# Kernel optimization log

Measured on AMD Instinct MI355X. Metric: run time of the kernel, lower is better.

The kernel has to match this reference:

```python
import jax, jax.numpy as jnp
import numpy as np

B, S, D, P = 4, 2048, 1024, 1024

def setup_inputs() -> dict:
    key = jax.random.key(0)
    k1, k2, k3, k4 = jax.random.split(key, 4)
    x = jax.random.normal(k1, (B, S, D), dtype=jnp.float32)
    # nn.Linear weight is (out, in); store transposed (in, out) for x @ W
    scale = 1.0 / np.sqrt(D)
    Wq = jax.random.normal(k2, (D, P), dtype=jnp.float32) * scale
    Wk = jax.random.normal(k3, (D, P), dtype=jnp.float32) * scale
    Wv = jax.random.normal(k4, (D, P), dtype=jnp.float32) * scale
    return {"x": x, "Wq": Wq, "Wk": Wk, "Wv": Wv}

def reference(x, Wq, Wk, Wv):
    # projections (no bias)
    q = x @ Wq  # (B,S,P)
    k = x @ Wk
    v = x @ Wv
    scores = jnp.einsum('bsd,btd->bst', q, k)  # (B,S,S)
    seq = x.shape[1]
    causal = jnp.triu(jnp.ones((seq, seq), dtype=bool), k=1)
    scores = jnp.where(causal, -jnp.inf, scores)
    scores = scores / jnp.sqrt(jnp.asarray(P, dtype=scores.dtype))
    attn = jax.nn.softmax(scores, axis=-1)
    # dropout_prob=0.0 -> identity
    context = jnp.einsum('bst,btd->bsd', attn, v)  # (B,S,P)
    return context
```

## Files before the change

kernel.cpp:

```cpp
#include <hip/hip_runtime.h>
#include <hip/hip_bf16.h>


#define BDIM 4
#define SDIM 2048
#define DDIM 1024
#define PDIM 1024

typedef __attribute__((ext_vector_type(8))) short bf16x8;
typedef __attribute__((ext_vector_type(4))) float f32x4;

__device__ __forceinline__ unsigned short f2bf(float f) {
    union { float f; unsigned int u; } v; v.f = f;
    unsigned int u = v.u;
    unsigned int r = (u + 0x7fffu + ((u >> 16) & 1u)) >> 16;
    return (unsigned short)r;
}

__device__ __forceinline__ float bf2f(unsigned short h) {
    union { unsigned int u; float f; } v;
    v.u = ((unsigned int)h) << 16;
    return v.f;
}

__device__ __forceinline__ void async16(const unsigned short* g, unsigned short* l) {
    __builtin_amdgcn_global_load_lds(
        (const __attribute__((address_space(1))) unsigned int*)g,
        (__attribute__((address_space(3))) unsigned int*)l,
        16, 0, 0);
}

__device__ __forceinline__ void storeC(float* C, size_t idx, float v) { C[idx] = v; }
__device__ __forceinline__ void storeC(unsigned short* C, size_t idx, float v) { C[idx] = f2bf(v); }

__global__ __launch_bounds__(256) void cast_x_kernel(const float* __restrict__ x,
                                                     unsigned short* __restrict__ y) {
    int i = blockIdx.x * 256 + threadIdx.x;
    float4 v = ((const float4*)x)[i];
    ushort4 o;
    o.x = f2bf(v.x); o.y = f2bf(v.y); o.z = f2bf(v.z); o.w = f2bf(v.w);
    ((ushort4*)y)[i] = o;
}

__global__ __launch_bounds__(256) void transpose_cast_w(const float* __restrict__ W0,
                                                        const float* __restrict__ W1,
                                                        const float* __restrict__ W2,
                                                        unsigned short* __restrict__ T) {
    const float* W = (blockIdx.z == 0) ? W0 : (blockIdx.z == 1) ? W1 : W2;
    unsigned short* Tz = T + (size_t)blockIdx.z * DDIM * PDIM;
    __shared__ float t[32][33];
    int c0 = blockIdx.x * 32, r0 = blockIdx.y * 32;
    for (int i = threadIdx.y; i < 32; i += 8)
        t[i][threadIdx.x] = W[(size_t)(r0 + i) * PDIM + c0 + threadIdx.x];
    __syncthreads();
    for (int i = threadIdx.y; i < 32; i += 8)
        Tz[(size_t)(c0 + i) * DDIM + r0 + threadIdx.x] = f2bf(t[threadIdx.x][i]);
}

template <int LDA, int LDB, int LDC, int KMAX, int MODE, typename CT>
__global__ __launch_bounds__(256) void gemm_bt(
    const unsigned short* __restrict__ A0, const unsigned short* __restrict__ A1,
    long long sA,
    const unsigned short* __restrict__ B0, long long sB,
    CT* __restrict__ C0, CT* __restrict__ C1, long long sC,
    unsigned short* __restrict__ Kb, unsigned short* __restrict__ VT,
    float alpha) {
    const int BM = 128, BN = 128, BK = 64;
    __shared__ __attribute__((aligned(16))) unsigned short smem[BM * BK + BN * BK];
    unsigned short* As = smem;
    unsigned short* Bs = smem + BM * BK;

    int tm, tn;
    if (MODE == 1) {
        int i = blockIdx.x;
        int t = (int)((sqrtf(8.f * i + 1.f) - 1.f) * 0.5f);
        if ((t + 1) * (t + 2) / 2 <= i) t++;
        if (t * (t + 1) / 2 > i) t--;
        tm = t * BM;
        tn = (i - t * (t + 1) / 2) * BN;
    } else {
        tm = blockIdx.y * BM;
        tn = blockIdx.x * BN;
    }
    int kend = (MODE == 2) ? min(KMAX, tm + BM) : KMAX;

    int z = blockIdx.z;
    const unsigned short* A = (z < 2 ? A0 : A1) + (long long)(z & 1) * sA;
    const unsigned short* Bt = B0 + (long long)z * sB;
    CT* C = (z < 2 ? C0 : C1) + (long long)(z & 1) * sC;

    int tid  = threadIdx.x;
    int lane = tid & 63;
    int wave = tid >> 6;
    int wr   = (wave >> 1) * 64;
    int wc   = (wave & 1) * 64;
    int quad = lane >> 4;
    int l16  = lane & 15;
    int rsw  = l16 & 7;

    f32x4 acc[4][4] = {};

    int srow = tid >> 3;
    int scol = ((tid & 7) ^ (srow & 7)) * 8;
    const unsigned short* Ag = A + (size_t)(tm + srow) * LDA + scol;
    const unsigned short* Bg = Bt + (size_t)(tn + srow) * LDB + scol;
    unsigned short* la = As + tid * 8;
    unsigned short* lb = Bs + tid * 8;

    auto kstep = [&](int k0) {
        async16(Ag + k0, la);
        async16(Ag + k0 + 32 * LDA, la + 2048);
        async16(Ag + k0 + 64 * LDA, la + 4096);
        async16(Ag + k0 + 96 * LDA, la + 6144);
        async16(Bg + k0, lb);
        async16(Bg + k0 + 32 * LDB, lb + 2048);
        async16(Bg + k0 + 64 * LDB, lb + 4096);
        async16(Bg + k0 + 96 * LDB, lb + 6144);
        __syncthreads();

#pragma unroll
        for (int s = 0; s < 2; s++) {
            int chunk = ((s * 4 + quad) ^ rsw) * 8;
            bf16x8 af[4], bfr[4];
#pragma unroll
            for (int i = 0; i < 4; i++)
                af[i] = *(const bf16x8*)(As + (wr + i * 16 + l16) * BK + chunk);
#pragma unroll
            for (int j = 0; j < 4; j++)
                bfr[j] = *(const bf16x8*)(Bs + (wc + j * 16 + l16) * BK + chunk);
#pragma unroll
            for (int i = 0; i < 4; i++)
#pragma unroll
                for (int j = 0; j < 4; j++)
                    acc[i][j] = __builtin_amdgcn_mfma_f32_16x16x32_bf16(af[i], bfr[j], acc[i][j], 0, 0, 0);
        }
        __syncthreads();
    };

    if constexpr (MODE != 2) {
#pragma unroll
        for (int k0 = 0; k0 < KMAX; k0 += BK) kstep(k0);
    } else {
        for (int k0 = 0; k0 < kend; k0 += 2 * BK) { kstep(k0); kstep(k0 + BK); }
    }

    if constexpr (MODE == 0) {
        if (tn < 2048) {
            unsigned short* D = (tn < 1024 ? (unsigned short*)C0 : Kb);
            int cbase = tn & 1023;
#pragma unroll
            for (int i = 0; i < 4; i++) {
                int r0 = tm + wr + i * 16 + quad * 4;
#pragma unroll
                for (int j = 0; j < 4; j++) {
                    int c = cbase + wc + j * 16 + l16;
#pragma unroll
                    for (int rr = 0; rr < 4; rr++)
                        D[(size_t)(r0 + rr) * 1024 + c] = f2bf(acc[i][j][rr]);
                }
            }
        } else {
            int b = tm >> 11;
            int s0 = tm & 2047;
            unsigned short* VTb = VT + (size_t)b * (PDIM * SDIM)
                                     + (size_t)(tn - 2048) * SDIM + s0;
            const int TP = 136;
            unsigned short* T = smem;
#pragma unroll
            for (int p = 0; p < 4; p++) {
                int jbase = -1;
                if (wc == 0 && p == 0) jbase = 0;
                if (wc == 0 && p == 1) jbase = 2;
                if (wc == 64 && p == 2) jbase = 0;
                if (wc == 64 && p == 3) jbase = 2;
                if (jbase >= 0) {
#pragma unroll
                    for (int jj = 0; jj < 2; jj++) {
                        int j = jbase + jj;
                        int c = (wc + j * 16 + l16) - 32 * p;
#pragma unroll
                        for (int i = 0; i < 4; i++) {
                            int r = wr + i * 16 + quad * 4;
                            ushort4 w;
                            w.x = f2bf(acc[i][j][0]); w.y = f2bf(acc[i][j][1]);
                            w.z = f2bf(acc[i][j][2]); w.w = f2bf(acc[i][j][3]);
                            *(ushort4*)(T + c * TP + r) = w;
                        }
                    }
                }
                __syncthreads();
                {
                    int lr = tid >> 3;
                    int ck = (tid & 7) * 16;
                    bf16x8 u0 = *(const bf16x8*)(T + lr * TP + ck);
                    bf16x8 u1 = *(const bf16x8*)(T + lr * TP + ck + 8);
                    unsigned short* dst = VTb + (size_t)(32 * p + lr) * SDIM + ck;
                    *(bf16x8*)(dst) = u0;
                    *(bf16x8*)(dst + 8) = u1;
                }
                __syncthreads();
            }
        }
    } else {
#pragma unroll
        for (int i = 0; i < 4; i++) {
            int r0 = tm + wr + i * 16 + quad * 4;
#pragma unroll
            for (int j = 0; j < 4; j++) {
                int c = tn + wc + j * 16 + l16;
#pragma unroll
                for (int rr = 0; rr < 4; rr++) {
                    int r = r0 + rr;
                    float v = acc[i][j][rr] * alpha;
                    if (MODE == 1 && c > r) v = -1e30f;
                    storeC(C, (size_t)r * LDC + c, v);
                }
            }
        }
    }
}

__global__ __launch_bounds__(256) void softmax_causal(unsigned short* __restrict__ S01,
                                                      unsigned short* __restrict__ S23,
                                                      long long sS) {
    int row = blockIdx.x;
    int b = blockIdx.y;
    unsigned short* srow = (b < 2 ? S01 : S23) + (long long)(b & 1) * sS + (size_t)row * SDIM;
    int tid = threadIdx.x;
    int j0 = tid * 8;
    int valid = row + 1;
    __shared__ float red[4];

    bf16x8 v8 = *(const bf16x8*)(srow + j0);
    float f[8];
#pragma unroll
    for (int i = 0; i < 8; i++) f[i] = bf2f((unsigned short)v8[i]);

    float m = -1e30f;
#pragma unroll
    for (int i = 0; i < 8; i++) if (j0 + i < valid) m = fmaxf(m, f[i]);
#pragma unroll
    for (int o = 32; o; o >>= 1) m = fmaxf(m, __shfl_xor(m, o, 64));
    if ((tid & 63) == 0) red[tid >> 6] = m;
    __syncthreads();
    m = fmaxf(fmaxf(red[0], red[1]), fmaxf(red[2], red[3]));
    __syncthreads();

    float e[8];
    float l = 0.f;
#pragma unroll
    for (int i = 0; i < 8; i++) {
        e[i] = (j0 + i < valid) ? __expf(f[i] - m) : 0.f;
        l += e[i];
    }
#pragma unroll
    for (int o = 32; o; o >>= 1) l += __shfl_xor(l, o, 64);
    if ((tid & 63) == 0) red[tid >> 6] = l;
    __syncthreads();
    l = red[0] + red[1] + red[2] + red[3];
    float inv = 1.0f / l;

    bf16x8 o8;
#pragma unroll
    for (int i = 0; i < 8; i++) o8[i] = (short)f2bf(e[i] * inv);
    *(bf16x8*)(srow + j0) = o8;
}

extern "C" void kernel_launch(void* const* d_in, const int* in_sizes, int n_in,
                              void* d_out, int out_size, void* d_ws, size_t ws_size,
                              hipStream_t stream) {
    const float* x  = (const float*)d_in[0];
    const float* Wq = (const float*)d_in[1];
    const float* Wk = (const float*)d_in[2];
    const float* Wv = (const float*)d_in[3];
    float* out = (float*)d_out;

    const size_t MS = (size_t)BDIM * SDIM;
    const long long SS = (long long)SDIM * SDIM;
    char* ws = (char*)d_ws;
    size_t off = 0;
    unsigned short* Xb   = (unsigned short*)(ws + off);
    unsigned short* S01  = Xb;                          off += MS * DDIM * 2;
    unsigned short* WT   = (unsigned short*)(ws + off); off += 3ull * DDIM * PDIM * 2;
    unsigned short* Q    = (unsigned short*)(ws + off); off += MS * PDIM * 2;
    unsigned short* Kb   = (unsigned short*)(ws + off); off += MS * PDIM * 2;
    unsigned short* VT   = (unsigned short*)(ws + off); off += MS * PDIM * 2;
    unsigned short* S23  = (unsigned short*)(ws + off); off += 2ull * SS * 2;

    cast_x_kernel<<<(MS * DDIM) / 1024, 256, 0, stream>>>(x, Xb);

    transpose_cast_w<<<dim3(PDIM / 32, DDIM / 32, 3), dim3(32, 8), 0, stream>>>(Wq, Wk, Wv, WT);

    gemm_bt<DDIM, DDIM, PDIM, DDIM, 0, unsigned short>
        <<<dim3(3 * PDIM / 128, MS / 128, 1), 256, 0, stream>>>(
        Xb, Xb, 0, WT, 0, Q, Q, 0, Kb, VT, 1.0f);

    const long long sQ = (long long)SDIM * PDIM;
    const float alpha = 1.0f / 32.0f;

    gemm_bt<PDIM, PDIM, SDIM, PDIM, 1, unsigned short>
        <<<dim3(136, 1, BDIM), 256, 0, stream>>>(
        Q, Q + 2 * sQ, sQ, Kb, sQ, S01, S23, SS, nullptr, nullptr, alpha);

    softmax_causal<<<dim3(SDIM, BDIM), 256, 0, stream>>>(S01, S23, SS);

    const long long sOut = (long long)SDIM * PDIM;
    gemm_bt<SDIM, SDIM, PDIM, SDIM, 2, float>
        <<<dim3(PDIM / 128, SDIM / 128, BDIM), 256, 0, stream>>>(
        S01, S23, SS, VT, sQ, out, out + 2 * sOut, sOut, nullptr, nullptr, 1.0f);
}
```

Before: 235.0 us.

## Double-buffer GEMM LDS loads, fuse prep kernels, and skip masked softmax work

```diff
diff --git a/kernel.cpp b/kernel.cpp
--- a/kernel.cpp
+++ b/kernel.cpp
@@ -33,28 +33,38 @@
 __device__ __forceinline__ void storeC(float* C, size_t idx, float v) { C[idx] = v; }
 __device__ __forceinline__ void storeC(unsigned short* C, size_t idx, float v) { C[idx] = f2bf(v); }
 
-__global__ __launch_bounds__(256) void cast_x_kernel(const float* __restrict__ x,
-                                                     unsigned short* __restrict__ y) {
-    int i = blockIdx.x * 256 + threadIdx.x;
-    float4 v = ((const float4*)x)[i];
-    ushort4 o;
-    o.x = f2bf(v.x); o.y = f2bf(v.y); o.z = f2bf(v.z); o.w = f2bf(v.w);
-    ((ushort4*)y)[i] = o;
-}
-
-__global__ __launch_bounds__(256) void transpose_cast_w(const float* __restrict__ W0,
-                                                        const float* __restrict__ W1,
-                                                        const float* __restrict__ W2,
-                                                        unsigned short* __restrict__ T) {
-    const float* W = (blockIdx.z == 0) ? W0 : (blockIdx.z == 1) ? W1 : W2;
-    unsigned short* Tz = T + (size_t)blockIdx.z * DDIM * PDIM;
-    __shared__ float t[32][33];
-    int c0 = blockIdx.x * 32, r0 = blockIdx.y * 32;
-    for (int i = threadIdx.y; i < 32; i += 8)
-        t[i][threadIdx.x] = W[(size_t)(r0 + i) * PDIM + c0 + threadIdx.x];
-    __syncthreads();
-    for (int i = threadIdx.y; i < 32; i += 8)
-        Tz[(size_t)(c0 + i) * DDIM + r0 + threadIdx.x] = f2bf(t[threadIdx.x][i]);
+__global__ __launch_bounds__(256) void prep_kernel(const float* __restrict__ x,
+                                                   const float* __restrict__ W0,
+                                                   const float* __restrict__ W1,
+                                                   const float* __restrict__ W2,
+                                                   unsigned short* __restrict__ Xb,
+                                                   unsigned short* __restrict__ WT) {
+    int bid = blockIdx.x;
+    if (bid < 4096) {
+        size_t i = (size_t)bid * 256 + threadIdx.x;
+        float4 a = ((const float4*)x)[2 * i];
+        float4 b = ((const float4*)x)[2 * i + 1];
+        bf16x8 o;
+        o[0] = (short)f2bf(a.x); o[1] = (short)f2bf(a.y);
+        o[2] = (short)f2bf(a.z); o[3] = (short)f2bf(a.w);
+        o[4] = (short)f2bf(b.x); o[5] = (short)f2bf(b.y);
+        o[6] = (short)f2bf(b.z); o[7] = (short)f2bf(b.w);
+        ((bf16x8*)Xb)[i] = o;
+    } else {
+        int idx = bid - 4096;
+        int wz = idx >> 10;
+        int t = idx & 1023;
+        const float* W = (wz == 0) ? W0 : (wz == 1) ? W1 : W2;
+        unsigned short* Tz = WT + (size_t)wz * DDIM * PDIM;
+        __shared__ float tle[32][33];
+        int c0 = (t & 31) * 32, r0 = (t >> 5) * 32;
+        int tx = threadIdx.x & 31, ty = threadIdx.x >> 5;
+        for (int i = ty; i < 32; i += 8)
+            tle[i][tx] = W[(size_t)(r0 + i) * PDIM + c0 + tx];
+        __syncthreads();
+        for (int i = ty; i < 32; i += 8)
+            Tz[(size_t)(c0 + i) * DDIM + r0 + tx] = f2bf(tle[tx][i]);
+    }
 }
 
 template <int LDA, int LDB, int LDC, int KMAX, int MODE, typename CT>
@@ -66,9 +76,8 @@
     unsigned short* __restrict__ Kb, unsigned short* __restrict__ VT,
     float alpha) {
     const int BM = 128, BN = 128, BK = 64;
-    __shared__ __attribute__((aligned(16))) unsigned short smem[BM * BK + BN * BK];
-    unsigned short* As = smem;
-    unsigned short* Bs = smem + BM * BK;
+    const int BUF = BM * BK + BN * BK;
+    __shared__ __attribute__((aligned(16))) unsigned short smem[2 * BUF];
 
     int tm, tn;
     if (MODE == 1) {
@@ -104,10 +113,10 @@
     int scol = ((tid & 7) ^ (srow & 7)) * 8;
     const unsigned short* Ag = A + (size_t)(tm + srow) * LDA + scol;
     const unsigned short* Bg = Bt + (size_t)(tn + srow) * LDB + scol;
-    unsigned short* la = As + tid * 8;
-    unsigned short* lb = Bs + tid * 8;
-
-    auto kstep = [&](int k0) {
+
+    auto issue = [&](int k0, int buf) {
+        unsigned short* la = smem + buf * BUF + tid * 8;
+        unsigned short* lb = la + BM * BK;
         async16(Ag + k0, la);
         async16(Ag + k0 + 32 * LDA, la + 2048);
         async16(Ag + k0 + 64 * LDA, la + 4096);
@@ -116,8 +125,11 @@
         async16(Bg + k0 + 32 * LDB, lb + 2048);
         async16(Bg + k0 + 64 * LDB, lb + 4096);
         async16(Bg + k0 + 96 * LDB, lb + 6144);
-        __syncthreads();
-
+    };
+
+    auto compute = [&](int buf) {
+        const unsigned short* As = smem + buf * BUF;
+        const unsigned short* Bs = As + BM * BK;
 #pragma unroll
         for (int s = 0; s < 2; s++) {
             int chunk = ((s * 4 + quad) ^ rsw) * 8;
@@ -134,14 +146,25 @@
                 for (int j = 0; j < 4; j++)
                     acc[i][j] = __builtin_amdgcn_mfma_f32_16x16x32_bf16(af[i], bfr[j], acc[i][j], 0, 0, 0);
         }
-        __syncthreads();
     };
 
     if constexpr (MODE != 2) {
-#pragma unroll
-        for (int k0 = 0; k0 < KMAX; k0 += BK) kstep(k0);
+        constexpr int NS = KMAX / BK;
+        issue(0, 0);
+#pragma unroll
+        for (int i = 0; i < NS; i++) {
+            __syncthreads();
+            if (i + 1 < NS) issue((i + 1) * BK, (i + 1) & 1);
+            compute(i & 1);
+        }
     } else {
-        for (int k0 = 0; k0 < kend; k0 += 2 * BK) { kstep(k0); kstep(k0 + BK); }
+        int ns = kend / BK;
+        issue(0, 0);
+        for (int i = 0; i < ns; i++) {
+            __syncthreads();
+            if (i + 1 < ns) issue((i + 1) * BK, (i + 1) & 1);
+            compute(i & 1);
+        }
     }
 
     if constexpr (MODE == 0) {
@@ -166,6 +189,7 @@
                                      + (size_t)(tn - 2048) * SDIM + s0;
             const int TP = 136;
             unsigned short* T = smem;
+            __syncthreads();
 #pragma unroll
             for (int p = 0; p < 4; p++) {
                 int jbase = -1;
@@ -211,9 +235,8 @@
 #pragma unroll
                 for (int rr = 0; rr < 4; rr++) {
                     int r = r0 + rr;
-                    float v = acc[i][j][rr] * alpha;
-                    if (MODE == 1 && c > r) v = -1e30f;
-                    storeC(C, (size_t)r * LDC + c, v);
+                    if (MODE == 1 && c > r) continue;
+                    storeC(C, (size_t)r * LDC + c, acc[i][j][rr] * alpha);
                 }
             }
         }
@@ -229,16 +252,22 @@
     int tid = threadIdx.x;
     int j0 = tid * 8;
     int valid = row + 1;
+    int bound = ((row >> 7) + 1) << 7;
+    bool active = j0 < valid;
     __shared__ float red[4];
 
-    bf16x8 v8 = *(const bf16x8*)(srow + j0);
     float f[8];
-#pragma unroll
-    for (int i = 0; i < 8; i++) f[i] = bf2f((unsigned short)v8[i]);
+    if (active) {
+        bf16x8 v8 = *(const bf16x8*)(srow + j0);
+#pragma unroll
+        for (int i = 0; i < 8; i++) f[i] = bf2f((unsigned short)v8[i]);
+    }
 
     float m = -1e30f;
-#pragma unroll
-    for (int i = 0; i < 8; i++) if (j0 + i < valid) m = fmaxf(m, f[i]);
+    if (active) {
+#pragma unroll
+        for (int i = 0; i < 8; i++) if (j0 + i < valid) m = fmaxf(m, f[i]);
+    }
 #pragma unroll
     for (int o = 32; o; o >>= 1) m = fmaxf(m, __shfl_xor(m, o, 64));
     if ((tid & 63) == 0) red[tid >> 6] = m;
@@ -246,12 +275,14 @@
     m = fmaxf(fmaxf(red[0], red[1]), fmaxf(red[2], red[3]));
     __syncthreads();
 
-    float e[8];
+    float e[8] = {0.f, 0.f, 0.f, 0.f, 0.f, 0.f, 0.f, 0.f};
     float l = 0.f;
-#pragma unroll
-    for (int i = 0; i < 8; i++) {
-        e[i] = (j0 + i < valid) ? __expf(f[i] - m) : 0.f;
-        l += e[i];
+    if (active) {
+#pragma unroll
+        for (int i = 0; i < 8; i++) {
+            e[i] = (j0 + i < valid) ? __expf(f[i] - m) : 0.f;
+            l += e[i];
+        }
     }
 #pragma unroll
     for (int o = 32; o; o >>= 1) l += __shfl_xor(l, o, 64);
@@ -260,10 +291,12 @@
     l = red[0] + red[1] + red[2] + red[3];
     float inv = 1.0f / l;
 
-    bf16x8 o8;
-#pragma unroll
-    for (int i = 0; i < 8; i++) o8[i] = (short)f2bf(e[i] * inv);
-    *(bf16x8*)(srow + j0) = o8;
+    if (j0 < bound) {
+        bf16x8 o8;
+#pragma unroll
+        for (int i = 0; i < 8; i++) o8[i] = (short)f2bf(e[i] * inv);
+        *(bf16x8*)(srow + j0) = o8;
+    }
 }
 
 extern "C" void kernel_launch(void* const* d_in, const int* in_sizes, int n_in,
@@ -287,9 +320,7 @@
     unsigned short* VT   = (unsigned short*)(ws + off); off += MS * PDIM * 2;
     unsigned short* S23  = (unsigned short*)(ws + off); off += 2ull * SS * 2;
 
-    cast_x_kernel<<<(MS * DDIM) / 1024, 256, 0, stream>>>(x, Xb);
-
-    transpose_cast_w<<<dim3(PDIM / 32, DDIM / 32, 3), dim3(32, 8), 0, stream>>>(Wq, Wk, Wv, WT);
+    prep_kernel<<<4096 + 3072, 256, 0, stream>>>(x, Wq, Wk, Wv, Xb, WT);
 
     gemm_bt<DDIM, DDIM, PDIM, DDIM, 0, unsigned short>
         <<<dim3(3 * PDIM / 128, MS / 128, 1), 256, 0, stream>>>(
```

New measurement: 232.5 us. No clear change (-1.1%).
